# Performance work log

Measured on AMD Instinct MI355X. Metric: run time of the kernel, lower is better.

## Reference

```python
import jax, jax.numpy as jnp
import numpy as np

BIT = 64
NUM_TRAIN = 200000
BATCH = 256
NUM_CLASSES = 100
MAX_SAMPLE = 30          # max_SampleNum in original
ALPHA = 0.01             # config['alpha']
M = 2 * BIT              # self.m = 2 * bit


def setup_inputs() -> dict:
    key = jax.random.key(0)
    k1, k2, k3, k4, k5 = jax.random.split(key, 5)
    u = jax.random.normal(k1, (BATCH, BIT), dtype=jnp.float32)
    y = jax.random.randint(k2, (BATCH,), 0, NUM_CLASSES)
    # distinct scatter targets into the bank, like dataloader sample indices
    ind = jax.random.choice(k3, NUM_TRAIN, (BATCH,), replace=False)
    U = jax.random.normal(k4, (NUM_TRAIN, BIT), dtype=jnp.float32)
    Y = jax.random.randint(k5, (NUM_TRAIN,), 0, NUM_CLASSES).astype(jnp.float32)
    return {"u": u, "y": y, "ind": ind, "U": U, "Y": Y}


def reference(u, y, ind, U, Y):
    yf = y.astype(jnp.float32)
    # scatter update of the memory bank (u.data -> detached in original)
    U = U.at[ind].set(jax.lax.stop_gradient(u))
    Y = Y.at[ind].set(yf)

    # For each sample, the first MAX_SAMPLE ascending indices with Y == y[i]
    # (same as torch.where(self.Y == indx)[0][:max_SampleNum]).
    match = (Y[None, :] == yf[:, None])                       # (B, N)
    pos = jnp.arange(NUM_TRAIN, dtype=jnp.int32)
    # matched positions keep their index; unmatched get index + N -> sorted after
    key_mat = jnp.where(match, pos[None, :], pos[None, :] + NUM_TRAIN)  # (B, N)
    _, order = jax.lax.top_k(-key_mat, MAX_SAMPLE)            # (B, 30) ascending matched idx first
    count = jnp.minimum(match.sum(axis=1), MAX_SAMPLE)        # per-row pool size
    valid = (jnp.arange(MAX_SAMPLE)[None, :] < count[:, None]).reshape(-1)  # (B*30,)

    pool_idx = order.reshape(-1)                              # (P,) P = B*30
    U_pool = U[pool_idx]                                      # (P, bit)
    Y_pool = Y[pool_idx]                                      # (P,)

    # pairwise squared distance u vs pool
    dist = jnp.sum((u[:, None, :] - U_pool[None, :, :]) ** 2, axis=2)  # (B, P)
    mism = (yf[:, None] != Y_pool[None, :]).astype(jnp.float32)        # (B, P)
    pair = (1.0 - mism) * 0.5 * dist + mism * 0.5 * jnp.clip(M - dist, 0.0)

    vmask = valid.astype(jnp.float32)[None, :]
    step = jnp.sum(valid.astype(jnp.float32))                 # dynamic pool length in original
    loss1 = jnp.sum(pair * vmask) / (u.shape[0] * step)       # == loss.mean() over (B, step)
    loss2 = ALPHA * jnp.mean(jnp.abs(jnp.abs(u) - 1.0))
    return loss1 + loss2
```

## Files before the change

### kernel.cpp

```cpp
#include <hip/hip_runtime.h>

#define NTRAIN 200000
#define NB     256
#define BIT    64
#define MAXS   30
#define HALF   15
#define NCLS   100
#define CHUNK  4096
#define PERT   16
#define MVAL   128.0f
#define ALPHA  0.01f

__global__ __launch_bounds__(256) void dsh_class_kernel(
    const float* __restrict__ u, const int* __restrict__ y,
    const int* __restrict__ ind, const float* __restrict__ U,
    const float* __restrict__ Y,
    float* __restrict__ partial, int* __restrict__ cntw)
{
    __shared__ int   ovr[CHUNK];
    __shared__ float up_l[HALF * BIT];
    __shared__ int   ind_l[NB];
    __shared__ int   y_l[NB];
    __shared__ int   pool[MAXS];
    __shared__ int   povr[MAXS];
    __shared__ int   wsum[4];
    __shared__ float red[4];

    const int t    = threadIdx.x;
    const int c    = blockIdx.x;
    const int h    = blockIdx.y;
    const int lane = t & 63;
    const int wave = t >> 6;

    ind_l[t] = ind[t];
    y_l[t]   = y[t];
    __syncthreads();

    unsigned long long bal = __ballot(y_l[t] == c);
    if (lane == 0) wsum[wave] = (int)__popcll(bal);
    __syncthreads();
    const int mult = wsum[0] + wsum[1] + wsum[2] + wsum[3];
    __syncthreads();
    if (mult == 0) {
        if (t == 0) {
            partial[c * 2 + h] = 0.f;
            if (h == 0) cntw[c] = 0;
        }
        return;
    }

    const float cf = (float)c;

    int count = 0;
    for (int base = 0; base < NTRAIN && count < MAXS; base += CHUNK) {
        #pragma unroll
        for (int k = 0; k < 4; ++k)
            ((int4*)ovr)[t + 256 * k] = make_int4(-1, -1, -1, -1);
        __syncthreads();
        unsigned rel = (unsigned)(ind_l[t] - base);
        if (rel < (unsigned)CHUNK) ovr[rel] = t;
        __syncthreads();

        const int s = base + t * PERT;
        int mbits = 0, mcnt = 0;
        if (s < NTRAIN) {
            float4 yv[4];
            const float4* yp = (const float4*)(Y + s);
            #pragma unroll
            for (int q = 0; q < 4; ++q) yv[q] = yp[q];
            const float* yf = (const float*)yv;
            #pragma unroll
            for (int k = 0; k < PERT; ++k) {
                int o = ovr[t * PERT + k];
                float yj = (o >= 0) ? (float)y_l[o] : yf[k];
                if (yj == cf) { mbits |= (1 << k); ++mcnt; }
            }
        }
        int x = mcnt;
        #pragma unroll
        for (int off = 1; off < 64; off <<= 1) {
            int v = __shfl_up(x, off, 64);
            if (lane >= off) x += v;
        }
        if (lane == 63) wsum[wave] = x;
        __syncthreads();
        int wpre = 0;
        #pragma unroll
        for (int w = 0; w < 4; ++w) if (w < wave) wpre += wsum[w];
        int r = count + wpre + (x - mcnt);
        #pragma unroll
        for (int k = 0; k < PERT; ++k) {
            if ((mbits >> k) & 1) {
                if (r < MAXS) pool[r] = s + k;
                ++r;
            }
        }
        count += wsum[0] + wsum[1] + wsum[2] + wsum[3];
        __syncthreads();
    }
    const int cnt = (count < MAXS) ? count : MAXS;

    if (t < MAXS) povr[t] = -1;
    __syncthreads();
    for (int k = 0; k < cnt; ++k)
        if (ind_l[t] == pool[k]) povr[k] = t;
    __syncthreads();

    const int p0 = h * HALF;
    const int pe = (h == 0) ? ((cnt < HALF) ? cnt : HALF) : cnt;
    for (int idx = t; idx < HALF * BIT; idx += 256) {
        const int pp = p0 + (idx >> 6);
        const int d  = idx & 63;
        float v = 0.f;
        if (pp < pe) {
            const int ov = povr[pp];
            v = (ov >= 0) ? u[ov * BIT + d] : U[pool[pp] * BIT + d];
        }
        up_l[idx] = v;
    }
    __syncthreads();

    float4 ur[16];
    {
        const float4* urp = (const float4*)(u + t * BIT);
        #pragma unroll
        for (int q = 0; q < 16; ++q) ur[q] = urp[q];
    }
    const bool same = (y_l[t] == c);
    float acc = 0.f;
    for (int pp = p0; pp < pe; ++pp) {
        const float4* up = (const float4*)(up_l + (pp - p0) * BIT);
        float d0 = 0.f, d1 = 0.f, d2 = 0.f, d3 = 0.f;
        #pragma unroll
        for (int q = 0; q < 16; ++q) {
            float4 v = up[q];
            float a0 = ur[q].x - v.x; d0 += a0 * a0;
            float a1 = ur[q].y - v.y; d1 += a1 * a1;
            float a2 = ur[q].z - v.z; d2 += a2 * a2;
            float a3 = ur[q].w - v.w; d3 += a3 * a3;
        }
        const float dist = (d0 + d1) + (d2 + d3);
        acc += same ? dist : fmaxf(MVAL - dist, 0.f);
    }

    #pragma unroll
    for (int off = 32; off; off >>= 1) acc += __shfl_down(acc, off, 64);
    if (lane == 0) red[wave] = acc;
    __syncthreads();
    if (t == 0) {
        partial[c * 2 + h] = (float)mult * (red[0] + red[1] + red[2] + red[3]);
        if (h == 0) cntw[c] = mult * cnt;
    }
}

__global__ __launch_bounds__(256) void dsh_final_kernel(
    const float* __restrict__ u,
    const float* __restrict__ partial, const int* __restrict__ cntw,
    float* __restrict__ out)
{
    const int t = threadIdx.x;
    const int lane = t & 63, wave = t >> 6;
    __shared__ float redp[4], reda[4];
    __shared__ int   redc[4];

    float p = (t < 2 * NCLS) ? partial[t] : 0.f;
    int   c = (t < NCLS) ? cntw[t] : 0;
    float a = 0.f;
    #pragma unroll
    for (int k = 0; k < 16; ++k) {
        float4 v = ((const float4*)u)[t + 256 * k];
        a += fabsf(fabsf(v.x) - 1.0f) + fabsf(fabsf(v.y) - 1.0f)
           + fabsf(fabsf(v.z) - 1.0f) + fabsf(fabsf(v.w) - 1.0f);
    }
    #pragma unroll
    for (int off = 32; off; off >>= 1) {
        p += __shfl_down(p, off, 64);
        a += __shfl_down(a, off, 64);
        c += __shfl_down(c, off, 64);
    }
    if (lane == 0) { redp[wave] = p; reda[wave] = a; redc[wave] = c; }
    __syncthreads();
    if (t == 0) {
        float P = redp[0] + redp[1] + redp[2] + redp[3];
        float A = reda[0] + reda[1] + reda[2] + reda[3];
        int   S = redc[0] + redc[1] + redc[2] + redc[3];
        float loss1 = 0.5f * P / (256.0f * (float)S);
        float loss2 = ALPHA * (A * (1.0f / 16384.0f));
        out[0] = loss1 + loss2;
    }
}

extern "C" void kernel_launch(void* const* d_in, const int* in_sizes, int n_in,
                              void* d_out, int out_size, void* d_ws, size_t ws_size,
                              hipStream_t stream) {
    const float* u   = (const float*)d_in[0];
    const int*   y   = (const int*)d_in[1];
    const int*   ind = (const int*)d_in[2];
    const float* U   = (const float*)d_in[3];
    const float* Y   = (const float*)d_in[4];
    float* out = (float*)d_out;

    float* partial = (float*)d_ws;
    int*   cntw    = (int*)((char*)d_ws + 2 * NCLS * sizeof(float));

    dsh_class_kernel<<<dim3(NCLS, 2), dim3(256), 0, stream>>>(
        u, y, ind, U, Y, partial, cntw);
    dsh_final_kernel<<<dim3(1), dim3(256), 0, stream>>>(u, partial, cntw, out);
}
```

Measured before the change: 27.04 us.

## Split per-class pool work across eight blocks and move regularizer into extra blocks

The per-class grid goes from 2 blocks to 8, each handling up to 4 pool entries, and 16 extra blocks compute the |u|-1 regularizer partial sums so the final kernel only reduces partials. The override table is transposed so each thread's shared-memory reads are strided by 256 rather than by 16, avoiding bank conflicts, and the Y loads are issued before the table clear to overlap latency. The intent is more parallelism across CUs and less serial work in the single-block final kernel. The tradeoff is that the chunked class scan is now repeated by 8 blocks per class instead of 2, which adds redundant Y reads.

```diff
diff --git a/kernel.cpp b/kernel.cpp
--- a/kernel.cpp
+++ b/kernel.cpp
@@ -4,34 +4,51 @@
 #define NB     256
 #define BIT    64
 #define MAXS   30
-#define HALF   15
 #define NCLS   100
+#define ESPL   8
+#define EPB    4
 #define CHUNK  4096
 #define PERT   16
+#define NREG   16
 #define MVAL   128.0f
 #define ALPHA  0.01f
 
-__global__ __launch_bounds__(256) void dsh_class_kernel(
+__global__ __launch_bounds__(256) void dsh_main_kernel(
     const float* __restrict__ u, const int* __restrict__ y,
     const int* __restrict__ ind, const float* __restrict__ U,
     const float* __restrict__ Y,
     float* __restrict__ partial, int* __restrict__ cntw)
 {
-    __shared__ int   ovr[CHUNK];
-    __shared__ float up_l[HALF * BIT];
+    __shared__ int   ovrT[CHUNK];
+    __shared__ float up_l[EPB * BIT];
     __shared__ int   ind_l[NB];
     __shared__ int   y_l[NB];
     __shared__ int   pool[MAXS];
-    __shared__ int   povr[MAXS];
+    __shared__ int   povr[EPB];
     __shared__ int   wsum[4];
     __shared__ float red[4];
 
     const int t    = threadIdx.x;
-    const int c    = blockIdx.x;
-    const int h    = blockIdx.y;
+    const int j    = blockIdx.x;
     const int lane = t & 63;
     const int wave = t >> 6;
 
+    if (j >= NCLS * ESPL) {
+        const int q = j - NCLS * ESPL;
+        float4 v = ((const float4*)u)[q * 256 + t];
+        float a = fabsf(fabsf(v.x) - 1.f) + fabsf(fabsf(v.y) - 1.f)
+                + fabsf(fabsf(v.z) - 1.f) + fabsf(fabsf(v.w) - 1.f);
+        #pragma unroll
+        for (int off = 32; off; off >>= 1) a += __shfl_down(a, off, 64);
+        if (lane == 0) red[wave] = a;
+        __syncthreads();
+        if (t == 0) partial[j] = red[0] + red[1] + red[2] + red[3];
+        return;
+    }
+
+    const int c = j >> 3;
+    const int e = j & 7;
+
     ind_l[t] = ind[t];
     y_l[t]   = y[t];
     __syncthreads();
@@ -40,40 +57,39 @@
     if (lane == 0) wsum[wave] = (int)__popcll(bal);
     __syncthreads();
     const int mult = wsum[0] + wsum[1] + wsum[2] + wsum[3];
-    __syncthreads();
     if (mult == 0) {
-        if (t == 0) {
-            partial[c * 2 + h] = 0.f;
-            if (h == 0) cntw[c] = 0;
-        }
+        if (t == 0) { partial[j] = 0.f; if (e == 0) cntw[c] = 0; }
         return;
     }
+    __syncthreads();
 
     const float cf = (float)c;
 
     int count = 0;
     for (int base = 0; base < NTRAIN && count < MAXS; base += CHUNK) {
-        #pragma unroll
-        for (int k = 0; k < 4; ++k)
-            ((int4*)ovr)[t + 256 * k] = make_int4(-1, -1, -1, -1);
+        const int s = base + t * PERT;
+        float yf[PERT];
+        if (s < NTRAIN) {
+            #pragma unroll
+            for (int q2 = 0; q2 < 4; ++q2)
+                ((float4*)yf)[q2] = ((const float4*)(Y + s))[q2];
+        }
+        #pragma unroll
+        for (int k2 = 0; k2 < 4; ++k2)
+            ((int4*)ovrT)[t + 256 * k2] = make_int4(-1, -1, -1, -1);
         __syncthreads();
         unsigned rel = (unsigned)(ind_l[t] - base);
-        if (rel < (unsigned)CHUNK) ovr[rel] = t;
-        __syncthreads();
-
-        const int s = base + t * PERT;
-        int mbits = 0, mcnt = 0;
+        if (rel < (unsigned)CHUNK)
+            ovrT[(rel & 15) * 256 + (rel >> 4)] = t;
+        __syncthreads();
+
+        unsigned mbits = 0; int mcnt = 0;
         if (s < NTRAIN) {
-            float4 yv[4];
-            const float4* yp = (const float4*)(Y + s);
             #pragma unroll
-            for (int q = 0; q < 4; ++q) yv[q] = yp[q];
-            const float* yf = (const float*)yv;
-            #pragma unroll
-            for (int k = 0; k < PERT; ++k) {
-                int o = ovr[t * PERT + k];
-                float yj = (o >= 0) ? (float)y_l[o] : yf[k];
-                if (yj == cf) { mbits |= (1 << k); ++mcnt; }
+            for (int k2 = 0; k2 < PERT; ++k2) {
+                int o = ovrT[k2 * 256 + t];
+                bool m = (o >= 0) ? (y_l[o] == c) : (yf[k2] == cf);
+                if (m) { mbits |= (1u << k2); ++mcnt; }
             }
         }
         int x = mcnt;
@@ -89,9 +105,9 @@
         for (int w = 0; w < 4; ++w) if (w < wave) wpre += wsum[w];
         int r = count + wpre + (x - mcnt);
         #pragma unroll
-        for (int k = 0; k < PERT; ++k) {
-            if ((mbits >> k) & 1) {
-                if (r < MAXS) pool[r] = s + k;
+        for (int k2 = 0; k2 < PERT; ++k2) {
+            if ((mbits >> k2) & 1u) {
+                if (r < MAXS) pool[r] = s + k2;
                 ++r;
             }
         }
@@ -100,23 +116,22 @@
     }
     const int cnt = (count < MAXS) ? count : MAXS;
 
-    if (t < MAXS) povr[t] = -1;
-    __syncthreads();
-    for (int k = 0; k < cnt; ++k)
-        if (ind_l[t] == pool[k]) povr[k] = t;
-    __syncthreads();
-
-    const int p0 = h * HALF;
-    const int pe = (h == 0) ? ((cnt < HALF) ? cnt : HALF) : cnt;
-    for (int idx = t; idx < HALF * BIT; idx += 256) {
-        const int pp = p0 + (idx >> 6);
-        const int d  = idx & 63;
+    const int p0 = e * EPB;
+    const int pe = (p0 + EPB < cnt) ? p0 + EPB : cnt;
+    if (t < EPB) povr[t] = -1;
+    __syncthreads();
+    for (int k2 = p0; k2 < pe; ++k2)
+        if (ind_l[t] == pool[k2]) povr[k2 - p0] = t;
+    __syncthreads();
+    {
+        const int pp = t >> 6;
+        const int d  = t & 63;
         float v = 0.f;
-        if (pp < pe) {
+        if (p0 + pp < pe) {
             const int ov = povr[pp];
-            v = (ov >= 0) ? u[ov * BIT + d] : U[pool[pp] * BIT + d];
-        }
-        up_l[idx] = v;
+            v = (ov >= 0) ? u[ov * BIT + d] : U[pool[p0 + pp] * BIT + d];
+        }
+        up_l[t] = v;
     }
     __syncthreads();
 
@@ -124,20 +139,21 @@
     {
         const float4* urp = (const float4*)(u + t * BIT);
         #pragma unroll
-        for (int q = 0; q < 16; ++q) ur[q] = urp[q];
+        for (int q2 = 0; q2 < 16; ++q2) ur[q2] = urp[q2];
     }
     const bool same = (y_l[t] == c);
+    const int npool = pe - p0;
     float acc = 0.f;
-    for (int pp = p0; pp < pe; ++pp) {
-        const float4* up = (const float4*)(up_l + (pp - p0) * BIT);
+    for (int pp = 0; pp < npool; ++pp) {
+        const float4* up = (const float4*)(up_l + pp * BIT);
         float d0 = 0.f, d1 = 0.f, d2 = 0.f, d3 = 0.f;
         #pragma unroll
-        for (int q = 0; q < 16; ++q) {
-            float4 v = up[q];
-            float a0 = ur[q].x - v.x; d0 += a0 * a0;
-            float a1 = ur[q].y - v.y; d1 += a1 * a1;
-            float a2 = ur[q].z - v.z; d2 += a2 * a2;
-            float a3 = ur[q].w - v.w; d3 += a3 * a3;
+        for (int q2 = 0; q2 < 16; ++q2) {
+            float4 v = up[q2];
+            float a0 = ur[q2].x - v.x; d0 += a0 * a0;
+            float a1 = ur[q2].y - v.y; d1 += a1 * a1;
+            float a2 = ur[q2].z - v.z; d2 += a2 * a2;
+            float a3 = ur[q2].w - v.w; d3 += a3 * a3;
         }
         const float dist = (d0 + d1) + (d2 + d3);
         acc += same ? dist : fmaxf(MVAL - dist, 0.f);
@@ -148,13 +164,12 @@
     if (lane == 0) red[wave] = acc;
     __syncthreads();
     if (t == 0) {
-        partial[c * 2 + h] = (float)mult * (red[0] + red[1] + red[2] + red[3]);
-        if (h == 0) cntw[c] = mult * cnt;
+        partial[j] = (float)mult * (red[0] + red[1] + red[2] + red[3]);
+        if (e == 0) cntw[c] = mult * cnt;
     }
 }
 
 __global__ __launch_bounds__(256) void dsh_final_kernel(
-    const float* __restrict__ u,
     const float* __restrict__ partial, const int* __restrict__ cntw,
     float* __restrict__ out)
 {
@@ -163,30 +178,27 @@
     __shared__ float redp[4], reda[4];
     __shared__ int   redc[4];
 
-    float p = (t < 2 * NCLS) ? partial[t] : 0.f;
-    int   c = (t < NCLS) ? cntw[t] : 0;
-    float a = 0.f;
+    float p = 0.f, a = 0.f;
     #pragma unroll
-    for (int k = 0; k < 16; ++k) {
-        float4 v = ((const float4*)u)[t + 256 * k];
-        a += fabsf(fabsf(v.x) - 1.0f) + fabsf(fabsf(v.y) - 1.0f)
-           + fabsf(fabsf(v.z) - 1.0f) + fabsf(fabsf(v.w) - 1.0f);
-    }
+    for (int k = 0; k < 4; ++k) {
+        const int idx = t + 256 * k;
+        if (idx < NCLS * ESPL)            p += partial[idx];
+        else if (idx < NCLS * ESPL + NREG) a += partial[idx];
+    }
+    int cc = (t < NCLS) ? cntw[t] : 0;
     #pragma unroll
     for (int off = 32; off; off >>= 1) {
-        p += __shfl_down(p, off, 64);
-        a += __shfl_down(a, off, 64);
-        c += __shfl_down(c, off, 64);
-    }
-    if (lane == 0) { redp[wave] = p; reda[wave] = a; redc[wave] = c; }
+        p  += __shfl_down(p,  off, 64);
+        a  += __shfl_down(a,  off, 64);
+        cc += __shfl_down(cc, off, 64);
+    }
+    if (lane == 0) { redp[wave] = p; reda[wave] = a; redc[wave] = cc; }
     __syncthreads();
     if (t == 0) {
         float P = redp[0] + redp[1] + redp[2] + redp[3];
         float A = reda[0] + reda[1] + reda[2] + reda[3];
         int   S = redc[0] + redc[1] + redc[2] + redc[3];
-        float loss1 = 0.5f * P / (256.0f * (float)S);
-        float loss2 = ALPHA * (A * (1.0f / 16384.0f));
-        out[0] = loss1 + loss2;
+        out[0] = 0.5f * P / (256.0f * (float)S) + ALPHA * (A * (1.0f / 16384.0f));
     }
 }
 
@@ -201,9 +213,9 @@
     float* out = (float*)d_out;
 
     float* partial = (float*)d_ws;
-    int*   cntw    = (int*)((char*)d_ws + 2 * NCLS * sizeof(float));
-
-    dsh_class_kernel<<<dim3(NCLS, 2), dim3(256), 0, stream>>>(
+    int*   cntw    = (int*)((char*)d_ws + 4096);
+
+    dsh_main_kernel<<<dim3(NCLS * ESPL + NREG), dim3(256), 0, stream>>>(
         u, y, ind, U, Y, partial, cntw);
-    dsh_final_kernel<<<dim3(1), dim3(256), 0, stream>>>(u, partial, cntw, out);
+    dsh_final_kernel<<<dim3(1), dim3(256), 0, stream>>>(partial, cntw, out);
 }
```

Result: faster. 22.17 us (median of 2 runs) (-18.0%).
